# Kernel tuning notes

Hardware: AMD Instinct MI355X
Metric: run time of the kernel (lower is better)

## Reference

```python
import jax, jax.numpy as jnp
import numpy as np

NUM_HEADS = 4
NUM_GROUPS = 8
EPS = 1e-5


def setup_inputs() -> dict:
    key = jax.random.key(0)
    ks = jax.random.split(key, 4)
    B, C, H, W = 16, 512, 64, 64
    x = jax.random.normal(ks[0], (B, C, H, W), dtype=jnp.float32)
    norm_g = jnp.ones((C,), dtype=jnp.float32)
    norm_b = jnp.zeros((C,), dtype=jnp.float32)
    qkv_w = jax.random.normal(ks[1], (3 * C, C), dtype=jnp.float32) * (1.0 / np.sqrt(C))
    qkv_b = jnp.zeros((3 * C,), dtype=jnp.float32)
    proj_w = jax.random.normal(ks[2], (C, C), dtype=jnp.float32) * (1.0 / np.sqrt(C))
    proj_b = jnp.zeros((C,), dtype=jnp.float32)
    return {"x": x, "norm_g": norm_g, "norm_b": norm_b,
            "qkv_w": qkv_w, "qkv_b": qkv_b, "proj_w": proj_w, "proj_b": proj_b}


def _group_norm(x, g, b):
    B, C, H, W = x.shape
    xg = x.reshape(B, NUM_GROUPS, C // NUM_GROUPS, H, W)
    mean = xg.mean(axis=(2, 3, 4), keepdims=True)
    var = xg.var(axis=(2, 3, 4), keepdims=True)
    xn = ((xg - mean) * jax.lax.rsqrt(var + EPS)).reshape(B, C, H, W)
    return xn * g[None, :, None, None] + b[None, :, None, None]


def reference(x, norm_g, norm_b, qkv_w, qkv_b, proj_w, proj_b):
    B, C, H, W = x.shape
    d = C // NUM_HEADS
    scale = d ** (-0.5)
    xn = _group_norm(x, norm_g, norm_b)
    # 1x1 conv == channel GEMM
    qkv = jnp.einsum('oc,bchw->bohw', qkv_w, xn) + qkv_b[None, :, None, None]
    qkv = qkv.reshape(B, NUM_HEADS, 3 * d, H * W)
    q, k, v = qkv[:, :, :d], qkv[:, :, d:2 * d], qkv[:, :, 2 * d:]
    # Faithful to the original (degenerate) einsum: q's last axis is summed out
    attn = jnp.einsum('bnhq,bnhk->bnhk', q, k) * scale
    attn = jax.nn.softmax(attn, axis=-1)
    out = jnp.einsum('bnhk,bnhv->bnhv', attn, v)
    out = out.reshape(B, C, H, W)
    out = jnp.einsum('oc,bchw->bohw', proj_w, out) + proj_b[None, :, None, None]
    return out + x
```

## Files before the change

kernel.cpp:

```cpp
#include <hip/hip_runtime.h>

#define CC 512
#define SS 4096
#define GELEMS 262144

typedef __attribute__((ext_vector_type(8))) __bf16 bf16x8;
typedef __attribute__((ext_vector_type(4))) float f32x4;
typedef __attribute__((ext_vector_type(4))) unsigned short us4;
typedef __attribute__((ext_vector_type(8))) unsigned short us8;

__device__ __forceinline__ unsigned short f2bf(float f) {
  unsigned int u = __float_as_uint(f);
  u += 0x7fffu + ((u >> 16) & 1u);
  return (unsigned short)(u >> 16);
}
__device__ __forceinline__ int qrow(int cv) { return ((cv >> 7) * 384) + 256 + (cv & 127); }

__device__ __forceinline__ void gl_lds16(const void* g, void* l) {
  __builtin_amdgcn_global_load_lds((const __attribute__((address_space(1))) unsigned int*)g,
                                   (__attribute__((address_space(3))) unsigned int*)l, 16, 0, 0);
}

__global__ __launch_bounds__(256) void k_front(const float* __restrict__ x,
    const float* __restrict__ pw, const float* __restrict__ qw,
    unsigned short* __restrict__ xbft, float* __restrict__ part, float* __restrict__ mw) {
  __shared__ float red[8];
  __shared__ __align__(16) unsigned short Asb[64 * 32];
  __shared__ __align__(16) unsigned short Bsb[64 * 32];
  int t = threadIdx.x;
  if (blockIdx.x < 8192) {
    int bid = blockIdx.x;
    int b = bid >> 9, rem = bid & 511, ct = rem >> 6, st = rem & 63;
    int c0 = ct * 64, s0 = st * 64;
    int s_l = t & 63, c8i = t >> 6;
    const float* xp = x + ((size_t)(b * 512 + c0 + c8i * 16)) * SS + s0 + s_l;
    float v0[8], v1[8];
#pragma unroll
    for (int j = 0; j < 8; ++j) v0[j] = xp[(size_t)j * SS];
#pragma unroll
    for (int j = 0; j < 8; ++j) v1[j] = xp[(size_t)(j + 8) * SS];
    float sm = 0.f, sq = 0.f;
#pragma unroll
    for (int j = 0; j < 8; ++j) {
      sm += v0[j] + v1[j];
      sq += v0[j] * v0[j] + v1[j] * v1[j];
    }
#pragma unroll
    for (int off = 32; off; off >>= 1) { sm += __shfl_down(sm, off); sq += __shfl_down(sq, off); }
    if ((t & 63) == 0) { red[c8i] = sm; red[4 + c8i] = sq; }
    __syncthreads();
    if (t == 0) {
      int pidx = (b * 8 + ct) * 64 + st;
      part[pidx * 2] = red[0] + red[1] + red[2] + red[3];
      part[pidx * 2 + 1] = red[4] + red[5] + red[6] + red[7];
    }
    unsigned short* tb = xbft + ((size_t)(b * 64 + st)) * 32768;
    us8 o0, o1;
#pragma unroll
    for (int j = 0; j < 8; ++j) { o0[j] = f2bf(v0[j]); o1[j] = f2bf(v1[j]); }
    int jj = s_l >> 4, frr = s_l & 15;
    {
      int k8g = ct * 8 + c8i * 2;
      int kc = k8g >> 4, s8l = (k8g >> 2) & 3, fql = k8g & 3;
      *(us8*)&tb[kc * 8192 + (s8l * 4 + jj) * 512 + (fql * 16 + frr) * 8] = o0;
    }
    {
      int k8g = ct * 8 + c8i * 2 + 1;
      int kc = k8g >> 4, s8l = (k8g >> 2) & 3, fql = k8g & 3;
      *(us8*)&tb[kc * 8192 + (s8l * 4 + jj) * 512 + (fql * 16 + frr) * 8] = o1;
    }
  } else {
    int bb = blockIdx.x - 8192;
    int bm = (bb >> 3) * 64;
    int bn = (bb & 7) * 64;
    int w = t >> 6, l = t & 63;
    int wm = (w >> 1) * 32, wn = (w & 1) * 32;
    int fr = l & 15, fk = (l >> 4) * 8;
    f32x4 acc[2][2] = {};
    for (int k0 = 0; k0 < 512; k0 += 32) {
#pragma unroll
      for (int i = 0; i < 2; ++i) {
        int e = i * 256 + t;
        int row = e >> 3, f4 = e & 7;
        float4 v = *(const float4*)&pw[(size_t)(bm + row) * 512 + k0 + f4 * 4];
        us4 pk; pk[0] = f2bf(v.x); pk[1] = f2bf(v.y); pk[2] = f2bf(v.z); pk[3] = f2bf(v.w);
        *(us4*)&Asb[row * 32 + f4 * 4] = pk;
      }
#pragma unroll
      for (int i = 0; i < 2; ++i) {
        int e = i * 256 + t;
        int row = e >> 4, f4 = e & 15;
        float4 v = *(const float4*)&qw[(size_t)qrow(k0 + row) * 512 + bn + f4 * 4];
        Bsb[(f4 * 4 + 0) * 32 + row] = f2bf(v.x);
        Bsb[(f4 * 4 + 1) * 32 + row] = f2bf(v.y);
        Bsb[(f4 * 4 + 2) * 32 + row] = f2bf(v.z);
        Bsb[(f4 * 4 + 3) * 32 + row] = f2bf(v.w);
      }
      __syncthreads();
      bf16x8 a[2], bfr[2];
#pragma unroll
      for (int i = 0; i < 2; ++i) a[i] = *(const bf16x8*)&Asb[(wm + i * 16 + fr) * 32 + fk];
#pragma unroll
      for (int j = 0; j < 2; ++j) bfr[j] = *(const bf16x8*)&Bsb[(wn + j * 16 + fr) * 32 + fk];
#pragma unroll
      for (int i = 0; i < 2; ++i)
#pragma unroll
        for (int j = 0; j < 2; ++j)
          acc[i][j] = __builtin_amdgcn_mfma_f32_16x16x32_bf16(a[i], bfr[j], acc[i][j], 0, 0, 0);
      __syncthreads();
    }
#pragma unroll
    for (int i = 0; i < 2; ++i)
#pragma unroll
      for (int j = 0; j < 2; ++j)
#pragma unroll
        for (int r = 0; r < 4; ++r) {
          int row = bm + wm + i * 16 + (l >> 4) * 4 + r;
          int col = bn + wn + j * 16 + (l & 15);
          mw[(size_t)row * 512 + col] = acc[i][j][r];
        }
  }
}

__global__ __launch_bounds__(256) void k_prep(const float* __restrict__ part,
    const float* __restrict__ ng, const float* __restrict__ nb,
    const float* __restrict__ mw, const float* __restrict__ pw,
    const float* __restrict__ qb, const float* __restrict__ pb,
    unsigned short* __restrict__ mwa, float* __restrict__ bias2) {
  int t = threadIdx.x;
  __shared__ float S1[512], S2[512];
  __shared__ float ms[8], rs[8];
  int b = (blockIdx.x < 2048) ? (blockIdx.x >> 7) : ((blockIdx.x - 2048) >> 3);
  {
    int g = t >> 5, i = t & 31;
    const float* p = part + (size_t)(b * 8 + g) * 128;
    float S = p[i * 2] + p[(i + 32) * 2];
    float Q = p[i * 2 + 1] + p[(i + 32) * 2 + 1];
#pragma unroll
    for (int off = 16; off; off >>= 1) { S += __shfl_down(S, off, 32); Q += __shfl_down(Q, off, 32); }
    if (i == 0) {
      float mean = S * (1.f / 262144.f);
      float var = Q * (1.f / 262144.f) - mean * mean;
      ms[g] = mean; rs[g] = rsqrtf(var + 1e-5f);
    }
  }
  __syncthreads();
  if (blockIdx.x < 2048) {
    int r4 = (blockIdx.x & 127) * 4;
#pragma unroll
    for (int q = 0; q < 2; ++q) { int c = t + q * 256; S1[c] = rs[c >> 6] * ng[c]; }
    __syncthreads();
    int c2 = r4 + (t >> 6), c = (t & 63) * 8;
    const float4* mr = (const float4*)&mw[(size_t)c2 * 512 + c];
    float4 m0 = mr[0], m1 = mr[1];
    const float4* ar = (const float4*)&S1[c];
    float4 a0 = ar[0], a1 = ar[1];
    float v[8] = {m0.x*a0.x, m0.y*a0.y, m0.z*a0.z, m0.w*a0.w,
                  m1.x*a1.x, m1.y*a1.y, m1.z*a1.z, m1.w*a1.w};
    if (c2 >= c && c2 < c + 8) v[c2 - c] += 1.0f;
    us8 o;
#pragma unroll
    for (int j = 0; j < 8; ++j) o[j] = f2bf(v[j]);
    int wblk = c2 >> 6, i2 = (c2 >> 4) & 3, fr = c2 & 15;
    int step = c >> 5, fq = (c >> 3) & 3;
    size_t addr = ((((size_t)(b * 8 + wblk) * 4 + i2) * 16 + step) * 64 + (fq * 16 + fr)) * 8;
    *(us8*)&mwa[addr] = o;
  } else {
    int c2b = ((blockIdx.x - 2048) & 7) * 64;
    int w = t >> 6, l = t & 63;
#pragma unroll
    for (int q = 0; q < 2; ++q) {
      int c = t + q * 256;
      float A = rs[c >> 6] * ng[c];
      S1[c] = nb[c] - ms[c >> 6] * A;
      S2[c] = qb[qrow(c)];
    }
    __syncthreads();
    for (int it = 0; it < 16; ++it) {
      int c2 = c2b + w * 16 + it;
      const float4* pwr = (const float4*)&pw[(size_t)c2 * 512];
      const float4* mwr = (const float4*)&mw[(size_t)c2 * 512];
      float4 p0 = pwr[l * 2], p1 = pwr[l * 2 + 1];
      float4 m0 = mwr[l * 2], m1 = mwr[l * 2 + 1];
      const float4* qs = (const float4*)&S2[l * 8];
      const float4* bs = (const float4*)&S1[l * 8];
      float4 q0 = qs[0], q1 = qs[1], b0 = bs[0], b1 = bs[1];
      float acc = p0.x * q0.x + p0.y * q0.y + p0.z * q0.z + p0.w * q0.w
                + p1.x * q1.x + p1.y * q1.y + p1.z * q1.z + p1.w * q1.w
                + m0.x * b0.x + m0.y * b0.y + m0.z * b0.z + m0.w * b0.w
                + m1.x * b1.x + m1.y * b1.y + m1.z * b1.z + m1.w * b1.w;
#pragma unroll
      for (int off = 32; off; off >>= 1) acc += __shfl_down(acc, off);
      if (l == 0) bias2[b * 512 + c2] = acc + pb[c2];
    }
  }
}

__global__ __launch_bounds__(512, 4) void k_fused5(const unsigned short* __restrict__ mwa,
    const unsigned short* __restrict__ xbft, const float* __restrict__ bias2,
    float* __restrict__ out) {
  __shared__ __align__(16) unsigned short Bs[2][8192];
  int bid0 = blockIdx.x;
  int bid = 1023 - ((bid0 & 7) * 128 + (bid0 >> 3));
  int b = bid >> 6, st = bid & 63;
  int s0 = st * 64;
  int t = threadIdx.x, w = t >> 6, l = t & 63;
  int m0 = w * 64;
  int fr = l & 15, fq = l >> 4;
  const unsigned short* tile = xbft + ((size_t)(b * 64 + st)) * 32768;
  const unsigned short* Ag = mwa + ((size_t)(b * 8 + w)) * 32768;

  auto stage = [&](int buf, int kc) {
    const unsigned short* src = tile + kc * 8192 + w * 1024 + l * 8;
    gl_lds16(src, &Bs[buf][w * 1024]);
    gl_lds16(src + 512, &Bs[buf][w * 1024 + 512]);
  };

  stage(0, 0);
  bf16x8 fa[2][4];
#pragma unroll
  for (int i = 0; i < 4; ++i)
    fa[0][i] = *(const bf16x8*)&Ag[(i * 16 + 0) * 512 + l * 8];
  __syncthreads();

  f32x4 acc[4][4] = {};
#pragma unroll
  for (int kc = 0; kc < 4; ++kc) {
    if (kc < 3) stage((kc + 1) & 1, kc + 1);
#pragma unroll
    for (int s8 = 0; s8 < 4; ++s8) {
      const int step = kc * 4 + s8;
      const int cur = step & 1;
      if (step < 15) {
#pragma unroll
        for (int i = 0; i < 4; ++i)
          fa[cur ^ 1][i] = *(const bf16x8*)&Ag[(i * 16 + step + 1) * 512 + l * 8];
      }
      bf16x8 fb[4];
#pragma unroll
      for (int j = 0; j < 4; ++j)
        fb[j] = *(const bf16x8*)&Bs[kc & 1][(s8 * 4 + j) * 512 + l * 8];
#pragma unroll
      for (int i = 0; i < 4; ++i)
#pragma unroll
        for (int j = 0; j < 4; ++j)
          acc[i][j] = __builtin_amdgcn_mfma_f32_16x16x32_bf16(fa[cur][i], fb[j], acc[i][j], 0, 0, 0);
    }
    if (kc < 3) __syncthreads();
  }

  float4 bi[4];
#pragma unroll
  for (int i = 0; i < 4; ++i)
    bi[i] = *(const float4*)&bias2[b * 512 + m0 + i * 16 + fq * 4];
  __syncthreads();
  float* Ls = (float*)Bs;
  float* ob = out + (size_t)b * 512 * SS + s0;
#pragma unroll
  for (int i = 0; i < 4; ++i) {
    float bir[4] = {bi[i].x, bi[i].y, bi[i].z, bi[i].w};
#pragma unroll
    for (int j = 0; j < 4; ++j)
#pragma unroll
      for (int r = 0; r < 4; ++r)
        Ls[w * 1024 + (fq * 4 + r) * 64 + (((j ^ fq) & 3) * 16 + fr)] = acc[i][j][r] + bir[r];
    asm volatile("s_waitcnt lgkmcnt(0)" ::: "memory");
    __builtin_amdgcn_sched_barrier(0);
#pragma unroll
    for (int q = 0; q < 4; ++q) {
      int row16 = q * 4 + (l >> 4);
      int colR = (l & 15) * 4;
      f32x4 v = *(const f32x4*)&Ls[w * 1024 + row16 * 64 + (colR ^ (q * 16))];
      __builtin_nontemporal_store(v, (f32x4*)&ob[(size_t)(m0 + i * 16 + row16) * SS + colR]);
    }
    asm volatile("s_waitcnt lgkmcnt(0)" ::: "memory");
  }
}

__global__ __launch_bounds__(256) void k_stats(const float* __restrict__ x, float* __restrict__ part) {
  int bid = blockIdx.x;
  int bg = bid >> 3, sp = bid & 7;
  const float4* p = (const float4*)(x + (size_t)bg * GELEMS + (size_t)sp * 32768);
  int t = threadIdx.x;
  float s = 0.f, ss = 0.f;
#pragma unroll
  for (int i = 0; i < 32; ++i) {
    float4 v = p[i * 256 + t];
    s += v.x + v.y + v.z + v.w;
    ss += v.x * v.x + v.y * v.y + v.z * v.z + v.w * v.w;
  }
#pragma unroll
  for (int off = 32; off; off >>= 1) { s += __shfl_down(s, off); ss += __shfl_down(ss, off); }
  __shared__ float red[8];
  int wid = t >> 6;
  if ((t & 63) == 0) { red[wid * 2] = s; red[wid * 2 + 1] = ss; }
  __syncthreads();
  if (t == 0) {
    part[bid * 2] = red[0] + red[2] + red[4] + red[6];
    part[bid * 2 + 1] = red[1] + red[3] + red[5] + red[7];
  }
}

__global__ __launch_bounds__(256) void k_mw(const float* __restrict__ pw, const float* __restrict__ qw,
                                            float* __restrict__ mw, unsigned short* __restrict__ mwbf) {
  __shared__ __align__(16) unsigned short Asb[64 * 32];
  __shared__ __align__(16) unsigned short Bsb[64 * 32];
  int t = threadIdx.x;
  int bm = (blockIdx.x >> 3) * 64;
  int bn = (blockIdx.x & 7) * 64;
  int w = t >> 6, l = t & 63;
  int wm = (w >> 1) * 32, wn = (w & 1) * 32;
  int fr = l & 15, fk = (l >> 4) * 8;
  f32x4 acc[2][2] = {};
  for (int k0 = 0; k0 < 512; k0 += 32) {
#pragma unroll
    for (int i = 0; i < 2; ++i) {
      int e = i * 256 + t;
      int row = e >> 3, f4 = e & 7;
      float4 v = *(const float4*)&pw[(size_t)(bm + row) * 512 + k0 + f4 * 4];
      us4 pk; pk[0] = f2bf(v.x); pk[1] = f2bf(v.y); pk[2] = f2bf(v.z); pk[3] = f2bf(v.w);
      *(us4*)&Asb[row * 32 + f4 * 4] = pk;
    }
#pragma unroll
    for (int i = 0; i < 2; ++i) {
      int e = i * 256 + t;
      int row = e >> 4, f4 = e & 15;
      float4 v = *(const float4*)&qw[(size_t)qrow(k0 + row) * 512 + bn + f4 * 4];
      Bsb[(f4 * 4 + 0) * 32 + row] = f2bf(v.x);
      Bsb[(f4 * 4 + 1) * 32 + row] = f2bf(v.y);
      Bsb[(f4 * 4 + 2) * 32 + row] = f2bf(v.z);
      Bsb[(f4 * 4 + 3) * 32 + row] = f2bf(v.w);
    }
    __syncthreads();
    bf16x8 a[2], bfr[2];
#pragma unroll
    for (int i = 0; i < 2; ++i) a[i] = *(const bf16x8*)&Asb[(wm + i * 16 + fr) * 32 + fk];
#pragma unroll
    for (int j = 0; j < 2; ++j) bfr[j] = *(const bf16x8*)&Bsb[(wn + j * 16 + fr) * 32 + fk];
#pragma unroll
    for (int i = 0; i < 2; ++i)
#pragma unroll
      for (int j = 0; j < 2; ++j)
        acc[i][j] = __builtin_amdgcn_mfma_f32_16x16x32_bf16(a[i], bfr[j], acc[i][j], 0, 0, 0);
    __syncthreads();
  }
#pragma unroll
  for (int i = 0; i < 2; ++i)
#pragma unroll
    for (int j = 0; j < 2; ++j)
#pragma unroll
      for (int r = 0; r < 4; ++r) {
        int row = bm + wm + i * 16 + (l >> 4) * 4 + r;
        int col = bn + wn + j * 16 + (l & 15);
        float v = acc[i][j][r];
        mw[(size_t)row * 512 + col] = v;
        mwbf[(size_t)row * 512 + col] = f2bf(v);
      }
}

__global__ __launch_bounds__(256) void k_fin(const float* __restrict__ part,
    const float* __restrict__ ng, const float* __restrict__ nb,
    float* __restrict__ afac, float* __restrict__ bcv, int np) {
  int b = blockIdx.x, t = threadIdx.x;
  __shared__ float mean_s[8], rstd_s[8];
  int g = t >> 5, i = t & 31;
  float S = 0.f, Q = 0.f;
  for (int k = i; k < np; k += 32) {
    S += part[((b * 8 + g) * np + k) * 2];
    Q += part[((b * 8 + g) * np + k) * 2 + 1];
  }
#pragma unroll
  for (int off = 16; off; off >>= 1) { S += __shfl_down(S, off, 32); Q += __shfl_down(Q, off, 32); }
  if (i == 0) {
    float mean = S * (1.f / 262144.f);
    float var = Q * (1.f / 262144.f) - mean * mean;
    mean_s[g] = mean;
    rstd_s[g] = rsqrtf(var + 1e-5f);
  }
  __syncthreads();
#pragma unroll
  for (int q = 0; q < 2; ++q) {
    int c = t + q * 256;
    int gg = c >> 6;
    float A = rstd_s[gg] * ng[c];
    afac[b * 512 + c] = A;
    bcv[b * 512 + c] = nb[c] - mean_s[gg] * A;
  }
}

__global__ __launch_bounds__(256) void k_bias2(const float* __restrict__ mw,
    const float* __restrict__ bcv, const float* __restrict__ pw,
    const float* __restrict__ qb, const float* __restrict__ pb, float* __restrict__ bias2) {
  int b = blockIdx.x >> 3, c2b = (blockIdx.x & 7) * 64;
  int t = threadIdx.x, w = t >> 6, l = t & 63;
  __shared__ float Bcs[512], Qbs[512];
  for (int i = t; i < 512; i += 256) { Bcs[i] = bcv[b * 512 + i]; Qbs[i] = qb[qrow(i)]; }
  __syncthreads();
  for (int it = 0; it < 16; ++it) {
    int c2 = c2b + w * 16 + it;
    const float4* pwr = (const float4*)&pw[(size_t)c2 * 512];
    const float4* mwr = (const float4*)&mw[(size_t)c2 * 512];
    float4 p0 = pwr[l * 2], p1 = pwr[l * 2 + 1];
    float4 m0 = mwr[l * 2], m1 = mwr[l * 2 + 1];
    const float4* qs = (const float4*)&Qbs[l * 8];
    const float4* bs = (const float4*)&Bcs[l * 8];
    float4 q0 = qs[0], q1 = qs[1], b0 = bs[0], b1 = bs[1];
    float acc = p0.x * q0.x + p0.y * q0.y + p0.z * q0.z + p0.w * q0.w
              + p1.x * q1.x + p1.y * q1.y + p1.z * q1.z + p1.w * q1.w
              + m0.x * b0.x + m0.y * b0.y + m0.z * b0.z + m0.w * b0.w
              + m1.x * b1.x + m1.y * b1.y + m1.z * b1.z + m1.w * b1.w;
#pragma unroll
    for (int off = 32; off; off >>= 1) acc += __shfl_down(acc, off);
    if (l == 0) bias2[b * 512 + c2] = acc + pb[c2];
  }
}

__global__ __launch_bounds__(256) void k_gemm_fb(const unsigned short* __restrict__ mwbf,
    const float* __restrict__ x, const float* __restrict__ afac,
    const float* __restrict__ bias2, float* __restrict__ out) {
  __shared__ __align__(16) unsigned short Ab[128 * 32];
  __shared__ __align__(16) unsigned short Bb[128 * 32];
  __shared__ float Afs[512];
  int bid0 = blockIdx.x;
  int bid = (bid0 & 7) * 256 + (bid0 >> 3);
  int b = bid >> 7, rem = bid & 127, nt = rem >> 2, mt = rem & 3;
  int m0 = mt * 128, s0 = nt * 128;
  int t = threadIdx.x, w = t >> 6, l = t & 63;
  int wm = (w >> 1) * 64, wn = (w & 1) * 64;
  const unsigned short* Ag = mwbf + (size_t)m0 * CC;
  int lr = l >> 2, lk = (l & 3) * 8;
  int fr = l & 15, fk = (l >> 4) * 8;
  for (int i = t; i < 512; i += 256) Afs[i] = afac[b * CC + i];
  __syncthreads();
  f32x4 acc[4][4] = {};
  for (int k0 = 0; k0 < CC; k0 += 32) {
#pragma unroll
    for (int q = 0; q < 2; ++q) {
      int row = w * 32 + q * 16;
      gl_lds16(Ag + (size_t)(row + lr) * CC + k0 + lk, &Ab[row * 32]);
    }
#pragma unroll
    for (int i2 = 0; i2 < 4; ++i2) {
      int e = i2 * 256 + t;
      int row = e >> 5, f4 = e & 31;
      float4 v = *(const float4*)&x[((size_t)(b * CC + k0 + row)) * SS + s0 + f4 * 4];
      float a = Afs[k0 + row];
      Bb[(f4 * 4 + 0) * 32 + row] = f2bf(v.x * a);
      Bb[(f4 * 4 + 1) * 32 + row] = f2bf(v.y * a);
      Bb[(f4 * 4 + 2) * 32 + row] = f2bf(v.z * a);
      Bb[(f4 * 4 + 3) * 32 + row] = f2bf(v.w * a);
    }
    __syncthreads();
    bf16x8 af[4], bfr[4];
#pragma unroll
    for (int i = 0; i < 4; ++i) af[i] = *(const bf16x8*)&Ab[(wm + i * 16 + fr) * 32 + fk];
#pragma unroll
    for (int j = 0; j < 4; ++j) bfr[j] = *(const bf16x8*)&Bb[(wn + j * 16 + fr) * 32 + fk];
#pragma unroll
    for (int i = 0; i < 4; ++i)
#pragma unroll
      for (int j = 0; j < 4; ++j)
        acc[i][j] = __builtin_amdgcn_mfma_f32_16x16x32_bf16(af[i], bfr[j], acc[i][j], 0, 0, 0);
    __syncthreads();
  }
  int c2b = m0 + wm, sb = s0 + wn;
  float bi[4][4];
#pragma unroll
  for (int i = 0; i < 4; ++i)
#pragma unroll
    for (int r = 0; r < 4; ++r)
      bi[i][r] = bias2[b * CC + c2b + i * 16 + (l >> 4) * 4 + r];
#pragma unroll
  for (int i = 0; i < 4; ++i)
#pragma unroll
    for (int j = 0; j < 4; ++j)
#pragma unroll
      for (int r = 0; r < 4; ++r) {
        int c2 = c2b + i * 16 + (l >> 4) * 4 + r;
        int s = sb + j * 16 + (l & 15);
        size_t oi = ((size_t)(b * CC + c2)) * SS + s;
        out[oi] = acc[i][j][r] + bi[i][r] + x[oi];
      }
}

extern "C" void kernel_launch(void* const* d_in, const int* in_sizes, int n_in,
                              void* d_out, int out_size, void* d_ws, size_t ws_size,
                              hipStream_t stream) {
  const float* x = (const float*)d_in[0];
  const float* ng = (const float*)d_in[1];
  const float* nb = (const float*)d_in[2];
  const float* qw = (const float*)d_in[3];
  const float* qb = (const float*)d_in[4];
  const float* pw = (const float*)d_in[5];
  const float* pb = (const float*)d_in[6];
  float* out = (float*)d_out;
  char* ws = (char*)d_ws;

  float* part = (float*)(ws + 0);
  float* afac = (float*)(ws + 65536);
  float* bcv = (float*)(ws + 98304);
  float* bias2 = (float*)(ws + 131072);
  float* mw = (float*)(ws + 163840);
  unsigned short* mwbf = (unsigned short*)(ws + 1212416);
  unsigned short* mwa = (unsigned short*)(ws + 1736704);
  unsigned short* xbft = (unsigned short*)(ws + 10125312);

  bool fast = ws_size >= 77234176ull;

  if (fast) {
    k_front<<<8256, 256, 0, stream>>>(x, pw, qw, xbft, part, mw);
    k_prep<<<2176, 256, 0, stream>>>(part, ng, nb, mw, pw, qb, pb, mwa, bias2);
    k_fused5<<<1024, 512, 0, stream>>>(mwa, xbft, bias2, out);
  } else {
    k_stats<<<1024, 256, 0, stream>>>(x, part);
    k_mw<<<64, 256, 0, stream>>>(pw, qw, mw, mwbf);
    k_fin<<<16, 256, 0, stream>>>(part, ng, nb, afac, bcv, 8);
    k_bias2<<<128, 256, 0, stream>>>(mw, bcv, pw, qb, pb, bias2);
    k_gemm_fb<<<2048, 256, 0, stream>>>(mwbf, x, afac, bias2, out);
  }
}
```

Baseline: 121.5 us.

## Drop bf16 x staging buffer; convert x in the GEMM kernel directly

The front kernel no longer writes a bf16 copy of x to the workspace. It now only computes group-norm partial sums using contiguous float4 loads, one block per eighth of a group. The fused GEMM kernel reads fp32 x itself, converts it to bf16, and stores the full 64-column K tile (64 KB) in LDS up front, replacing the double-buffered async LDS staging. This removes a 64 MB write plus a 64 MB read of the intermediate. The cost is that x is read twice, a larger LDS footprint with occupancy lowered from 4 to 2, and no overlap between loading and MFMA work in the GEMM.

```diff
diff --git a/kernel.cpp b/kernel.cpp
--- a/kernel.cpp
+++ b/kernel.cpp
@@ -23,57 +23,35 @@
 
 __global__ __launch_bounds__(256) void k_front(const float* __restrict__ x,
     const float* __restrict__ pw, const float* __restrict__ qw,
-    unsigned short* __restrict__ xbft, float* __restrict__ part, float* __restrict__ mw) {
+    float* __restrict__ part, float* __restrict__ mw) {
   __shared__ float red[8];
   __shared__ __align__(16) unsigned short Asb[64 * 32];
   __shared__ __align__(16) unsigned short Bsb[64 * 32];
   int t = threadIdx.x;
-  if (blockIdx.x < 8192) {
+  int w = t >> 6, l = t & 63;
+  if (blockIdx.x < 1024) {
     int bid = blockIdx.x;
-    int b = bid >> 9, rem = bid & 511, ct = rem >> 6, st = rem & 63;
-    int c0 = ct * 64, s0 = st * 64;
-    int s_l = t & 63, c8i = t >> 6;
-    const float* xp = x + ((size_t)(b * 512 + c0 + c8i * 16)) * SS + s0 + s_l;
-    float v0[8], v1[8];
-#pragma unroll
-    for (int j = 0; j < 8; ++j) v0[j] = xp[(size_t)j * SS];
-#pragma unroll
-    for (int j = 0; j < 8; ++j) v1[j] = xp[(size_t)(j + 8) * SS];
-    float sm = 0.f, sq = 0.f;
-#pragma unroll
-    for (int j = 0; j < 8; ++j) {
-      sm += v0[j] + v1[j];
-      sq += v0[j] * v0[j] + v1[j] * v1[j];
-    }
-#pragma unroll
-    for (int off = 32; off; off >>= 1) { sm += __shfl_down(sm, off); sq += __shfl_down(sq, off); }
-    if ((t & 63) == 0) { red[c8i] = sm; red[4 + c8i] = sq; }
+    int bg = bid >> 3, sp = bid & 7;
+    const float4* p = (const float4*)(x + (size_t)bg * GELEMS + (size_t)sp * 32768);
+    float s = 0.f, ss = 0.f;
+#pragma unroll
+    for (int i = 0; i < 32; ++i) {
+      float4 v = p[i * 256 + t];
+      s += v.x + v.y + v.z + v.w;
+      ss += v.x * v.x + v.y * v.y + v.z * v.z + v.w * v.w;
+    }
+#pragma unroll
+    for (int off = 32; off; off >>= 1) { s += __shfl_down(s, off); ss += __shfl_down(ss, off); }
+    if (l == 0) { red[w * 2] = s; red[w * 2 + 1] = ss; }
     __syncthreads();
     if (t == 0) {
-      int pidx = (b * 8 + ct) * 64 + st;
-      part[pidx * 2] = red[0] + red[1] + red[2] + red[3];
-      part[pidx * 2 + 1] = red[4] + red[5] + red[6] + red[7];
-    }
-    unsigned short* tb = xbft + ((size_t)(b * 64 + st)) * 32768;
-    us8 o0, o1;
-#pragma unroll
-    for (int j = 0; j < 8; ++j) { o0[j] = f2bf(v0[j]); o1[j] = f2bf(v1[j]); }
-    int jj = s_l >> 4, frr = s_l & 15;
-    {
-      int k8g = ct * 8 + c8i * 2;
-      int kc = k8g >> 4, s8l = (k8g >> 2) & 3, fql = k8g & 3;
-      *(us8*)&tb[kc * 8192 + (s8l * 4 + jj) * 512 + (fql * 16 + frr) * 8] = o0;
-    }
-    {
-      int k8g = ct * 8 + c8i * 2 + 1;
-      int kc = k8g >> 4, s8l = (k8g >> 2) & 3, fql = k8g & 3;
-      *(us8*)&tb[kc * 8192 + (s8l * 4 + jj) * 512 + (fql * 16 + frr) * 8] = o1;
+      part[bid * 2] = red[0] + red[2] + red[4] + red[6];
+      part[bid * 2 + 1] = red[1] + red[3] + red[5] + red[7];
     }
   } else {
-    int bb = blockIdx.x - 8192;
+    int bb = blockIdx.x - 1024;
     int bm = (bb >> 3) * 64;
     int bn = (bb & 7) * 64;
-    int w = t >> 6, l = t & 63;
     int wm = (w >> 1) * 32, wn = (w & 1) * 32;
     int fr = l & 15, fk = (l >> 4) * 8;
     f32x4 acc[2][2] = {};
@@ -133,9 +111,9 @@
   int b = (blockIdx.x < 2048) ? (blockIdx.x >> 7) : ((blockIdx.x - 2048) >> 3);
   {
     int g = t >> 5, i = t & 31;
-    const float* p = part + (size_t)(b * 8 + g) * 128;
-    float S = p[i * 2] + p[(i + 32) * 2];
-    float Q = p[i * 2 + 1] + p[(i + 32) * 2 + 1];
+    const float* p = part + ((size_t)(b * 8 + g)) * 16;
+    float S = 0.f, Q = 0.f;
+    if (i < 8) { S = p[i * 2]; Q = p[i * 2 + 1]; }
 #pragma unroll
     for (int off = 16; off; off >>= 1) { S += __shfl_down(S, off, 32); Q += __shfl_down(Q, off, 32); }
     if (i == 0) {
@@ -196,10 +174,10 @@
   }
 }
 
-__global__ __launch_bounds__(512, 4) void k_fused5(const unsigned short* __restrict__ mwa,
-    const unsigned short* __restrict__ xbft, const float* __restrict__ bias2,
+__global__ __launch_bounds__(512, 2) void k_fused6(const unsigned short* __restrict__ mwa,
+    const float* __restrict__ x, const float* __restrict__ bias2,
     float* __restrict__ out) {
-  __shared__ __align__(16) unsigned short Bs[2][8192];
+  __shared__ __align__(16) unsigned short Bt[32768];
   int bid0 = blockIdx.x;
   int bid = 1023 - ((bid0 & 7) * 128 + (bid0 >> 3));
   int b = bid >> 6, st = bid & 63;
@@ -207,16 +185,22 @@
   int t = threadIdx.x, w = t >> 6, l = t & 63;
   int m0 = w * 64;
   int fr = l & 15, fq = l >> 4;
-  const unsigned short* tile = xbft + ((size_t)(b * 64 + st)) * 32768;
   const unsigned short* Ag = mwa + ((size_t)(b * 8 + w)) * 32768;
 
-  auto stage = [&](int buf, int kc) {
-    const unsigned short* src = tile + kc * 8192 + w * 1024 + l * 8;
-    gl_lds16(src, &Bs[buf][w * 1024]);
-    gl_lds16(src + 512, &Bs[buf][w * 1024 + 512]);
-  };
-
-  stage(0, 0);
+  const float* xb = x + ((size_t)b * 512) * SS + s0 + l;
+#pragma unroll
+  for (int i = 0; i < 8; ++i) {
+    int g = i * 8 + w;
+    int kc = g >> 4, s8l = (g >> 2) & 3, fql = g & 3;
+    const float* src = xb + (size_t)(g * 8) * SS;
+    float e[8];
+#pragma unroll
+    for (int j = 0; j < 8; ++j) e[j] = src[(size_t)j * SS];
+    us8 o;
+#pragma unroll
+    for (int j = 0; j < 8; ++j) o[j] = f2bf(e[j]);
+    *(us8*)&Bt[kc * 8192 + (s8l * 4 + (l >> 4)) * 512 + (fql * 16 + (l & 15)) * 8] = o;
+  }
   bf16x8 fa[2][4];
 #pragma unroll
   for (int i = 0; i < 4; ++i)
@@ -225,28 +209,22 @@
 
   f32x4 acc[4][4] = {};
 #pragma unroll
-  for (int kc = 0; kc < 4; ++kc) {
-    if (kc < 3) stage((kc + 1) & 1, kc + 1);
-#pragma unroll
-    for (int s8 = 0; s8 < 4; ++s8) {
-      const int step = kc * 4 + s8;
-      const int cur = step & 1;
-      if (step < 15) {
-#pragma unroll
-        for (int i = 0; i < 4; ++i)
-          fa[cur ^ 1][i] = *(const bf16x8*)&Ag[(i * 16 + step + 1) * 512 + l * 8];
-      }
-      bf16x8 fb[4];
+  for (int step = 0; step < 16; ++step) {
+    const int cur = step & 1;
+    if (step < 15) {
+#pragma unroll
+      for (int i = 0; i < 4; ++i)
+        fa[cur ^ 1][i] = *(const bf16x8*)&Ag[(i * 16 + step + 1) * 512 + l * 8];
+    }
+    bf16x8 fb[4];
+#pragma unroll
+    for (int j = 0; j < 4; ++j)
+      fb[j] = *(const bf16x8*)&Bt[(step >> 2) * 8192 + ((step & 3) * 4 + j) * 512 + l * 8];
+#pragma unroll
+    for (int i = 0; i < 4; ++i)
 #pragma unroll
       for (int j = 0; j < 4; ++j)
-        fb[j] = *(const bf16x8*)&Bs[kc & 1][(s8 * 4 + j) * 512 + l * 8];
-#pragma unroll
-      for (int i = 0; i < 4; ++i)
-#pragma unroll
-        for (int j = 0; j < 4; ++j)
-          acc[i][j] = __builtin_amdgcn_mfma_f32_16x16x32_bf16(fa[cur][i], fb[j], acc[i][j], 0, 0, 0);
-    }
-    if (kc < 3) __syncthreads();
+        acc[i][j] = __builtin_amdgcn_mfma_f32_16x16x32_bf16(fa[cur][i], fb[j], acc[i][j], 0, 0, 0);
   }
 
   float4 bi[4];
@@ -254,7 +232,7 @@
   for (int i = 0; i < 4; ++i)
     bi[i] = *(const float4*)&bias2[b * 512 + m0 + i * 16 + fq * 4];
   __syncthreads();
-  float* Ls = (float*)Bs;
+  float* Ls = (float*)Bt;
   float* ob = out + (size_t)b * 512 * SS + s0;
 #pragma unroll
   for (int i = 0; i < 4; ++i) {
@@ -503,14 +481,13 @@
   float* mw = (float*)(ws + 163840);
   unsigned short* mwbf = (unsigned short*)(ws + 1212416);
   unsigned short* mwa = (unsigned short*)(ws + 1736704);
-  unsigned short* xbft = (unsigned short*)(ws + 10125312);
-
-  bool fast = ws_size >= 77234176ull;
+
+  bool fast = ws_size >= 10125312ull;
 
   if (fast) {
-    k_front<<<8256, 256, 0, stream>>>(x, pw, qw, xbft, part, mw);
+    k_front<<<1088, 256, 0, stream>>>(x, pw, qw, part, mw);
     k_prep<<<2176, 256, 0, stream>>>(part, ng, nb, mw, pw, qb, pb, mwa, bias2);
-    k_fused5<<<1024, 512, 0, stream>>>(mwa, xbft, bias2, out);
+    k_fused6<<<1024, 512, 0, stream>>>(mwa, x, bias2, out);
   } else {
     k_stats<<<1024, 256, 0, stream>>>(x, part);
     k_mw<<<64, 256, 0, stream>>>(pw, qw, mw, mwbf);
```

Measured after the change: 120.5 us. About the same (-0.9%).
